# Performance work log

Hardware: AMD Instinct MI355X
Metric: run time of the kernel (lower is better)

## Reference

```python
import jax, jax.numpy as jnp
import numpy as np

EMBED_DIM = 1024
ZDIM = 128
STD = 0.02


def setup_inputs() -> dict:
    key = jax.random.key(0)
    ks = jax.random.split(key, 12)
    T, S, B, E, Z = 2048, 2048, 4, EMBED_DIM, ZDIM
    return {
        "query": jax.random.normal(ks[0], (T, B, E), jnp.float32),
        "key": jax.random.normal(ks[1], (S, B, E), jnp.float32),
        "Wq": jax.random.normal(ks[2], (2 * E + Z, E), jnp.float32) * STD,
        "bq": jnp.zeros((2 * E + Z,), jnp.float32),
        "Wk": jax.random.normal(ks[3], (Z, E), jnp.float32) * STD,
        "bk": jnp.zeros((Z,), jnp.float32),
        "Wv": jax.random.normal(ks[4], (E, E), jnp.float32) * STD,
        "bv": jnp.zeros((E,), jnp.float32),
        "Wh": jax.random.normal(ks[5], (E, E), jnp.float32) * STD,
        "bh": jnp.zeros((E,), jnp.float32),
        "gamma": jax.random.normal(ks[6], (2, Z), jnp.float32) * STD,
        "beta": jnp.zeros((2, Z), jnp.float32),
    }


def reference(query, key, Wq, bq, Wk, bk, Wv, bv, Wh, bh, gamma, beta):
    E, Z = EMBED_DIM, ZDIM
    scaling = Z ** (-0.5)
    # base: [T, B, 2E+Z]
    base = jnp.einsum('tbe,fe->tbf', query, Wq) + bq
    u = jax.nn.sigmoid(base[..., :E])                      # [T,B,E] output gate
    rq = jax.nn.silu(base[..., E:])                        # [T,B,E+Z]
    r = rq[..., :E]                                        # [T,B,E]
    q = rq[..., E:] * gamma[0] + beta[0]                   # [T,B,Z]
    k = jax.nn.silu(jnp.einsum('sbe,ze->sbz', key, Wk) + bk) * gamma[1] + beta[1]  # [S,B,Z]
    v = jax.nn.silu(jnp.einsum('sbe,fe->sbf', key, Wv) + bv)                       # [S,B,E]
    # softmax attention over context dim
    qk = jnp.einsum('tbz,sbz->bts', q * scaling, k)        # [B,T,S]
    attn = jax.nn.softmax(qk, axis=-1)
    h = jnp.einsum('bts,sbf->tbf', attn, v)                # [T,B,E]
    h = jnp.tanh(jnp.einsum('tbe,fe->tbf', h * r, Wh) + bh)
    out = query + u * (h - query)                          # addcmul
    return out
```

## Files before the change

### kernel.cpp

```cpp
#include <hip/hip_runtime.h>
#include <cstdint>
#include <cstddef>

using short8  = __attribute__((ext_vector_type(8))) short;
using floatx4 = __attribute__((ext_vector_type(4))) float;

#define DEV __device__ __forceinline__

DEV float u2f(unsigned short u){
  union { unsigned int i; float f; } c; c.i = ((unsigned int)u) << 16; return c.f;
}
DEV unsigned short f2u(float f){
  union { float f; unsigned int i; } c; c.f = f;
  unsigned int i = c.i;
  i += 0x7fffu + ((i >> 16) & 1u);
  return (unsigned short)(i >> 16);
}
DEV float sigmoidf_(float x){ return 1.0f / (1.0f + __expf(-x)); }
DEV float siluf_(float x){ return x / (1.0f + __expf(-x)); }

#define ASYNC_LD16(g, l) __builtin_amdgcn_global_load_lds( \
    (const __attribute__((address_space(1))) unsigned int*)(g), \
    (__attribute__((address_space(3))) unsigned int*)(l), 16, 0, 0)

#define MFMA_BF16 __builtin_amdgcn_mfma_f32_16x16x32_bf16

#define SBAR() asm volatile("s_barrier" ::: "memory")

constexpr float SCALING = 0.088388347648318447f;

__global__ __launch_bounds__(256) void cast_act(
    const float* __restrict__ q, const float* __restrict__ k,
    unsigned short* __restrict__ qo, unsigned short* __restrict__ ko)
{
  const int bid = blockIdx.x;
  const int e = threadIdx.x * 4;
  const float* src; unsigned short* dst;
  if (bid < 8192) {
    src = q + (long long)bid * 1024;
    dst = qo + (long long)bid * 1024;
  } else {
    const int m = bid - 8192;
    const int s = m >> 2, b = m & 3;
    src = k + (long long)m * 1024;
    dst = ko + ((long long)b * 2048 + s) * 1024;
  }
  const float4 v = *(const float4*)(src + e);
  ushort4 o; o.x=f2u(v.x); o.y=f2u(v.y); o.z=f2u(v.z); o.w=f2u(v.w);
  *(ushort4*)(dst + e) = o;
}

__global__ __launch_bounds__(256) void cast_w(
    const float* __restrict__ Wq, const float* __restrict__ Wk,
    const float* __restrict__ Wv, const float* __restrict__ Wh,
    unsigned short* __restrict__ oq, unsigned short* __restrict__ ok,
    unsigned short* __restrict__ ov, unsigned short* __restrict__ oh)
{
  const int bid = blockIdx.x;
  const int e = threadIdx.x * 4;
  const float* src; unsigned short* dst;
  if (bid < 2176)      { src = Wq + (long long)bid * 1024;        dst = oq + (long long)bid * 1024; }
  else if (bid < 2304) { src = Wk + (long long)(bid-2176) * 1024; dst = ok + (long long)(bid-2176) * 1024; }
  else if (bid < 3328) { src = Wv + (long long)(bid-2304) * 1024; dst = ov + (long long)(bid-2304) * 1024; }
  else                 { src = Wh + (long long)(bid-3328) * 1024; dst = oh + (long long)(bid-3328) * 1024; }
  const float4 v = *(const float4*)(src + e);
  ushort4 o; o.x=f2u(v.x); o.y=f2u(v.y); o.z=f2u(v.z); o.w=f2u(v.w);
  *(ushort4*)(dst + e) = o;
}

template<int EPI>
__global__ __launch_bounds__(256, 2)
void gemm_bt(const unsigned short* __restrict__ A, long long bsA, int lda,
             const unsigned short* __restrict__ Bm, long long bsB, int ldb,
             int K,
             const float* __restrict__ bias,
             const float* __restrict__ gam,
             const float* __restrict__ bet,
             float* __restrict__ f0,
             unsigned short* __restrict__ b0,
             unsigned short* __restrict__ b1,
             const unsigned short* __restrict__ rmul,
             const float* __restrict__ qin)
{
  __shared__ __align__(16) unsigned short As[128][64];
  __shared__ __align__(16) unsigned short Bs[128][64];

  const int tid = threadIdx.x;
  const int bm = blockIdx.x, bn = blockIdx.y, bz = blockIdx.z;
  const unsigned short* Ag = A  + (long long)bz * bsA;
  const unsigned short* Bg = Bm + (long long)bz * bsB;
  const int row0 = bm * 128;
  const int col0 = bn * 128;

  const int lane = tid & 63;
  const int wv   = tid >> 6;
  const int wm   = (wv & 1) * 64;
  const int wn   = (wv >> 1) * 64;
  const int lr   = lane & 15;
  const int lq   = lane >> 4;
  const int r7   = lr & 7;

  const unsigned short* gA[4]; const unsigned short* gB[4];
  unsigned short* lA[4]; unsigned short* lB[4];
  #pragma unroll
  for (int i = 0; i < 4; i++) {
    const int c  = tid + i * 256;
    const int rr = c >> 3;
    const int gc = (c & 7) ^ (rr & 7);
    gA[i] = Ag + (long long)(row0 + rr) * lda + gc * 8;
    gB[i] = Bg + (long long)(col0 + rr) * ldb + gc * 8;
    lA[i] = &As[0][0] + c * 8;
    lB[i] = &Bs[0][0] + c * 8;
  }

  floatx4 acc[4][4];
  const floatx4 zero = {0.f, 0.f, 0.f, 0.f};
  #pragma unroll
  for (int i = 0; i < 4; i++)
    #pragma unroll
    for (int j = 0; j < 4; j++) acc[i][j] = zero;

  for (int kt = 0; kt < K; kt += 64) {
    #pragma unroll
    for (int i = 0; i < 4; i++) {
      ASYNC_LD16(gA[i] + kt, lA[i]);
      ASYNC_LD16(gB[i] + kt, lB[i]);
    }
    __syncthreads();
    #pragma unroll
    for (int ks = 0; ks < 64; ks += 32) {
      const int k8 = ks >> 3;
      short8 af[4], bfv[4];
      #pragma unroll
      for (int i = 0; i < 4; i++) {
        const int sc = (lq + k8) ^ r7;
        af[i]  = *(const short8*)(&As[wm + i*16 + lr][sc * 8]);
        bfv[i] = *(const short8*)(&Bs[wn + i*16 + lr][sc * 8]);
      }
      #pragma unroll
      for (int mi = 0; mi < 4; mi++)
        #pragma unroll
        for (int ni = 0; ni < 4; ni++)
          acc[mi][ni] = MFMA_BF16(af[mi], bfv[ni], acc[mi][ni], 0, 0, 0);
    }
    __syncthreads();
  }

  #pragma unroll
  for (int mi = 0; mi < 4; mi++) {
    float s4[4];
    float iv[4];
    if constexpr (EPI == 3) {
      #pragma unroll
      for (int r = 0; r < 4; r++) s4[r] = 0.f;
    }
    if constexpr (EPI == 4) {
      #pragma unroll
      for (int r = 0; r < 4; r++) {
        const int gm = row0 + wm + mi * 16 + lq * 4 + r;
        iv[r] = 1.0f / f0[(long long)bz * 2048 + gm];
      }
    }
    #pragma unroll
    for (int ni = 0; ni < 4; ni++) {
      #pragma unroll
      for (int r = 0; r < 4; r++) {
        const int gm = row0 + wm + mi * 16 + lq * 4 + r;
        const int gn = col0 + wn + ni * 16 + lr;
        float v = acc[mi][ni][r];
        if constexpr (EPI == 2) {
          v += bias[gm];
          const int b = gn >> 11, s = gn & 2047;
          b0[((long long)b * 1024 + gm) * 2048 + s] = f2u(siluf_(v));
        } else if constexpr (EPI == 3) {
          const float e = __expf(v * SCALING);
          b0[(long long)bz * 2048 * 2048 + (long long)gm * 2048 + gn] = f2u(e);
          s4[r] += e;
        } else if constexpr (EPI == 4) {
          const long long idx = ((long long)gm * 4 + bz) * 1024 + gn;
          b0[idx] = f2u(v * iv[r] * u2f(rmul[idx]));
        } else {
          const long long idx = (long long)gm * 1024 + gn;
          const float tv = tanhf(v + bias[gn]);
          const float qv = qin[idx];
          f0[idx] = qv + u2f(rmul[idx]) * (tv - qv);
        }
      }
    }
    if constexpr (EPI == 3) {
      #pragma unroll
      for (int r = 0; r < 4; r++) {
        float s = s4[r];
        #pragma unroll
        for (int m2 = 8; m2 >= 1; m2 >>= 1) s += __shfl_xor(s, m2);
        if (lr == 0) {
          const int gm = row0 + wm + mi * 16 + lq * 4 + r;
          atomicAdd(f0 + (long long)bz * 2048 + gm, s);
        }
      }
    }
  }
}

__global__ __launch_bounds__(256, 2)
void gemm_nz128(const unsigned short* __restrict__ A0, const unsigned short* __restrict__ A1,
                const unsigned short* __restrict__ B0, const unsigned short* __restrict__ B1,
                const float* __restrict__ bi0, const float* __restrict__ bi1,
                const float* __restrict__ g0,  const float* __restrict__ g1,
                const float* __restrict__ be0, const float* __restrict__ be1,
                unsigned short* __restrict__ o0, unsigned short* __restrict__ o1)
{
  __shared__ __align__(16) unsigned short As[128][64];
  __shared__ __align__(16) unsigned short Bs[128][64];

  const int tid = threadIdx.x;
  const int bm = blockIdx.x;
  const int z  = blockIdx.z;
  const unsigned short* Ag = z ? A1 : A0;
  const unsigned short* Bg = z ? B1 : B0;
  const float* bias = z ? bi1 : bi0;
  const float* gam  = z ? g1  : g0;
  const float* bet  = z ? be1 : be0;
  unsigned short* ob = z ? o1 : o0;
  const int row0 = bm * 128;

  const int lane = tid & 63;
  const int wv   = tid >> 6;
  const int wm   = (wv & 1) * 64;
  const int wn   = (wv >> 1) * 64;
  const int lr   = lane & 15;
  const int lq   = lane >> 4;
  const int r7   = lr & 7;

  const unsigned short* gA[4]; const unsigned short* gB[4];
  unsigned short* lA[4]; unsigned short* lB[4];
  #pragma unroll
  for (int i = 0; i < 4; i++) {
    const int c  = tid + i * 256;
    const int rr = c >> 3;
    const int gc = (c & 7) ^ (rr & 7);
    gA[i] = Ag + (long long)(row0 + rr) * 1024 + gc * 8;
    gB[i] = Bg + (long long)rr * 1024 + gc * 8;
    lA[i] = &As[0][0] + c * 8;
    lB[i] = &Bs[0][0] + c * 8;
  }

  floatx4 acc[4][4];
  const floatx4 zero = {0.f, 0.f, 0.f, 0.f};
  #pragma unroll
  for (int i = 0; i < 4; i++)
    #pragma unroll
    for (int j = 0; j < 4; j++) acc[i][j] = zero;

  for (int kt = 0; kt < 1024; kt += 64) {
    #pragma unroll
    for (int i = 0; i < 4; i++) {
      ASYNC_LD16(gA[i] + kt, lA[i]);
      ASYNC_LD16(gB[i] + kt, lB[i]);
    }
    __syncthreads();
    #pragma unroll
    for (int ks = 0; ks < 64; ks += 32) {
      const int k8 = ks >> 3;
      short8 af[4], bfv[4];
      #pragma unroll
      for (int i = 0; i < 4; i++) {
        const int sc = (lq + k8) ^ r7;
        af[i]  = *(const short8*)(&As[wm + i*16 + lr][sc * 8]);
        bfv[i] = *(const short8*)(&Bs[wn + i*16 + lr][sc * 8]);
      }
      #pragma unroll
      for (int mi = 0; mi < 4; mi++)
        #pragma unroll
        for (int ni = 0; ni < 4; ni++)
          acc[mi][ni] = MFMA_BF16(af[mi], bfv[ni], acc[mi][ni], 0, 0, 0);
    }
    __syncthreads();
  }

  #pragma unroll
  for (int mi = 0; mi < 4; mi++)
    #pragma unroll
    for (int ni = 0; ni < 4; ni++)
      #pragma unroll
      for (int r = 0; r < 4; r++) {
        const int gm = row0 + wm + mi * 16 + lq * 4 + r;
        const int gn = wn + ni * 16 + lr;
        float v = acc[mi][ni][r] + bias[gn];
        ob[(long long)gm * 128 + gn] = f2u(siluf_(v) * gam[gn] + bet[gn]);
      }
}

__global__ __launch_bounds__(512, 2)
void gemm256(const unsigned short* __restrict__ A, int lda,
             const unsigned short* __restrict__ Bm, int ldb,
             int K,
             const float* __restrict__ bias,
             float* __restrict__ f0,
             unsigned short* __restrict__ b0)
{
  __shared__ __align__(16) unsigned short Ls[65536];

  const int tid = threadIdx.x;
  const int bm = blockIdx.x, bn = blockIdx.y;
  const int row0 = bm * 256;
  const int col0 = bn * 256;

  const int lane = tid & 63;
  const int wv   = tid >> 6;
  const int wr   = (wv >> 2) * 128;
  const int wc   = (wv & 3) * 64;
  const int lr   = lane & 15;
  const int lq   = lane >> 4;
  const int r7   = lr & 7;

  const int rr0 = tid >> 3;
  const int swz = ((tid & 7) ^ (rr0 & 7)) * 8;
  const unsigned short* gA0 = A  + (long long)(row0 + rr0) * lda + swz;
  const unsigned short* gB0 = Bm + (long long)(col0 + rr0) * ldb + swz;
  const long long sA64 = 64LL * lda, sB64 = 64LL * ldb;
  unsigned short* lA0 = &Ls[0]     + tid * 8;
  unsigned short* lB0 = &Ls[16384] + tid * 8;

  floatx4 acc[8][4];
  const floatx4 zero = {0.f, 0.f, 0.f, 0.f};
  #pragma unroll
  for (int i = 0; i < 8; i++)
    #pragma unroll
    for (int j = 0; j < 4; j++) acc[i][j] = zero;

  const int NT = K >> 6;

  #pragma unroll
  for (int i = 0; i < 4; i++) ASYNC_LD16(gA0 + i * sA64,      lA0 + i * 4096);
  #pragma unroll
  for (int i = 0; i < 4; i++) ASYNC_LD16(gB0 + i * sB64,      lB0 + i * 4096);
  #pragma unroll
  for (int i = 0; i < 4; i++) ASYNC_LD16(gA0 + i * sA64 + 64, lA0 + i * 4096 + 32768);
  #pragma unroll
  for (int i = 0; i < 4; i++) ASYNC_LD16(gB0 + i * sB64 + 64, lB0 + i * 4096 + 32768);
  asm volatile("s_waitcnt vmcnt(8)" ::: "memory");
  SBAR();

  for (int t = 0; t < NT; ++t) {
    const int cb = (t & 1) << 15;
    const unsigned short* Ab = &Ls[cb];
    const unsigned short* Bb = &Ls[cb + 16384];
    const bool st = (t + 2) < NT;
    const int kt2 = (t + 2) << 6;

    short8 afA[4][2], afB[4][2], bf01[2][2], bf23[2][2];

    #pragma unroll
    for (int mi = 0; mi < 4; mi++)
      #pragma unroll
      for (int k = 0; k < 2; k++)
        afA[mi][k] = *(const short8*)(Ab + (wr + mi*16 + lr) * 64 + (((k<<2) + lq) ^ r7) * 8);
    #pragma unroll
    for (int ni = 0; ni < 2; ni++)
      #pragma unroll
      for (int k = 0; k < 2; k++)
        bf01[ni][k] = *(const short8*)(Bb + (wc + ni*16 + lr) * 64 + (((k<<2) + lq) ^ r7) * 8);
    asm volatile("s_waitcnt lgkmcnt(8)" ::: "memory");
    SBAR();
    asm volatile("s_waitcnt lgkmcnt(0)" ::: "memory");
    __builtin_amdgcn_sched_barrier(0);
    __builtin_amdgcn_s_setprio(1);
    #pragma unroll
    for (int mi = 0; mi < 4; mi++)
      #pragma unroll
      for (int ni = 0; ni < 2; ni++)
        #pragma unroll
        for (int k = 0; k < 2; k++)
          acc[mi][ni] = MFMA_BF16(afA[mi][k], bf01[ni][k], acc[mi][ni], 0, 0, 0);
    __builtin_amdgcn_s_setprio(0);
    SBAR();

    #pragma unroll
    for (int ni = 0; ni < 2; ni++)
      #pragma unroll
      for (int k = 0; k < 2; k++)
        bf23[ni][k] = *(const short8*)(Bb + (wc + (ni+2)*16 + lr) * 64 + (((k<<2) + lq) ^ r7) * 8);
    SBAR();
    asm volatile("s_waitcnt lgkmcnt(0)" ::: "memory");
    __builtin_amdgcn_sched_barrier(0);
    __builtin_amdgcn_s_setprio(1);
    #pragma unroll
    for (int mi = 0; mi < 4; mi++)
      #pragma unroll
      for (int ni = 0; ni < 2; ni++)
        #pragma unroll
        for (int k = 0; k < 2; k++)
          acc[mi][ni+2] = MFMA_BF16(afA[mi][k], bf23[ni][k], acc[mi][ni+2], 0, 0, 0);
    __builtin_amdgcn_s_setprio(0);
    SBAR();

    #pragma unroll
    for (int mi = 0; mi < 4; mi++)
      #pragma unroll
      for (int k = 0; k < 2; k++)
        afB[mi][k] = *(const short8*)(Ab + (wr + (mi+4)*16 + lr) * 64 + (((k<<2) + lq) ^ r7) * 8);
    if (st) {
      #pragma unroll
      for (int i = 0; i < 4; i++) ASYNC_LD16(gB0 + i * sB64 + kt2, lB0 + i * 4096 + cb);
    }
    SBAR();
    asm volatile("s_waitcnt lgkmcnt(0)" ::: "memory");
    __builtin_amdgcn_sched_barrier(0);
    __builtin_amdgcn_s_setprio(1);
    #pragma unroll
    for (int mi = 0; mi < 4; mi++)
      #pragma unroll
      for (int ni = 0; ni < 2; ni++)
        #pragma unroll
        for (int k = 0; k < 2; k++)
          acc[mi+4][ni] = MFMA_BF16(afB[mi][k], bf01[ni][k], acc[mi+4][ni], 0, 0, 0);
    __builtin_amdgcn_s_setprio(0);
    SBAR();

    if (st) {
      #pragma unroll
      for (int i = 0; i < 4; i++) ASYNC_LD16(gA0 + i * sA64 + kt2, lA0 + i * 4096 + cb);
    }
    SBAR();
    __builtin_amdgcn_s_setprio(1);
    #pragma unroll
    for (int mi = 0; mi < 4; mi++)
      #pragma unroll
      for (int ni = 0; ni < 2; ni++)
        #pragma unroll
        for (int k = 0; k < 2; k++)
          acc[mi+4][ni+2] = MFMA_BF16(afB[mi][k], bf23[ni][k], acc[mi+4][ni+2], 0, 0, 0);
    __builtin_amdgcn_s_setprio(0);
    if (st) { asm volatile("s_waitcnt vmcnt(8)" ::: "memory"); }
    else    { asm volatile("s_waitcnt vmcnt(0)" ::: "memory"); }
    SBAR();
  }

  #pragma unroll
  for (int mi = 0; mi < 8; mi++)
    #pragma unroll
    for (int ni = 0; ni < 4; ni++)
      #pragma unroll
      for (int r = 0; r < 4; r++) {
        const int gm = row0 + wr + mi * 16 + lq * 4 + r;
        const int gn = col0 + wc + ni * 16 + lr;
        float v = acc[mi][ni][r] + bias[gn];
        if (gn < 1024) {
          ((unsigned short*)f0)[(long long)gm * 1024 + gn] = f2u(sigmoidf_(v));
        } else {
          b0[(long long)gm * 1024 + (gn - 1024)] = f2u(siluf_(v));
        }
      }
}

extern "C" void kernel_launch(void* const* d_in, const int* in_sizes, int n_in,
                              void* d_out, int out_size, void* d_ws, size_t ws_size,
                              hipStream_t stream)
{
  (void)in_sizes; (void)n_in; (void)out_size; (void)ws_size;
  const float* query = (const float*)d_in[0];
  const float* key   = (const float*)d_in[1];
  const float* Wq    = (const float*)d_in[2];
  const float* bq    = (const float*)d_in[3];
  const float* Wk    = (const float*)d_in[4];
  const float* bk    = (const float*)d_in[5];
  const float* Wv    = (const float*)d_in[6];
  const float* bv    = (const float*)d_in[7];
  const float* Wh    = (const float*)d_in[8];
  const float* bh    = (const float*)d_in[9];
  const float* gamma = (const float*)d_in[10];
  const float* beta  = (const float*)d_in[11];
  float* out = (float*)d_out;

  char* p = (char*)d_ws;
  auto take = [&](size_t bytes) -> char* {
    char* r = p; p += (bytes + 255) & ~(size_t)255; return r;
  };
  unsigned short* qbf = (unsigned short*)take(8192ULL * 1024 * 2);
  unsigned short* kbr = (unsigned short*)take(8192ULL * 1024 * 2);
  unsigned short* Wqb = (unsigned short*)take(2176ULL * 1024 * 2);
  unsigned short* Wkb = (unsigned short*)take(128ULL  * 1024 * 2);
  unsigned short* Wvb = (unsigned short*)take(1024ULL * 1024 * 2);
  unsigned short* Whb = (unsigned short*)take(1024ULL * 1024 * 2);
  unsigned short* ub  = (unsigned short*)take(8192ULL * 1024 * 2);
  unsigned short* rbf = (unsigned short*)take(8192ULL * 1024 * 2);
  unsigned short* qpj = (unsigned short*)take(8192ULL * 128 * 2);
  unsigned short* kpj = (unsigned short*)take(8192ULL * 128 * 2);
  unsigned short* vT  = (unsigned short*)take(4ULL * 1024 * 2048 * 2);
  unsigned short* Pb  = (unsigned short*)take(4ULL * 2048 * 2048 * 2);
  unsigned short* hrb = (unsigned short*)take(8192ULL * 1024 * 2);
  float*          rs  = (float*)take(4ULL * 2048 * 4);

  dim3 blk(256);
  dim3 gblk(512);
  cast_act<<<16384, blk, 0, stream>>>(query, key, qbf, kbr);
  cast_w<<<4352, blk, 0, stream>>>(Wq, Wk, Wv, Wh, Wqb, Wkb, Wvb, Whb);
  hipMemsetAsync(rs, 0, 4ULL * 2048 * 4, stream);

  gemm_nz128<<<dim3(64, 1, 2), blk, 0, stream>>>(
      qbf, kbr, Wqb + 2048LL * 1024, Wkb,
      bq + 2048, bk, gamma, gamma + 128, beta, beta + 128, qpj, kpj);
  gemm256<<<dim3(32, 8, 1), gblk, 0, stream>>>(qbf, 1024, Wqb, 1024, 1024,
      bq, (float*)ub, rbf);
  gemm_bt<2><<<dim3(8, 64, 1), blk, 0, stream>>>(Wvb, 0, 1024, kbr, 0, 1024, 1024,
      bv, nullptr, nullptr, nullptr, vT, nullptr, nullptr, nullptr);
  gemm_bt<3><<<dim3(16, 16, 4), blk, 0, stream>>>(qpj, 128, 512, kpj, 2048LL * 128, 128, 128,
      nullptr, nullptr, nullptr, rs, Pb, nullptr, nullptr, nullptr);
  gemm_bt<4><<<dim3(16, 8, 4), blk, 0, stream>>>(Pb, 2048LL * 2048, 2048,
      vT, 1024LL * 2048, 2048, 2048,
      nullptr, nullptr, nullptr, rs, hrb, nullptr, rbf, nullptr);
  gemm_bt<5><<<dim3(64, 8, 1), blk, 0, stream>>>(hrb, 0, 1024, Whb, 0, 1024, 1024,
      bh, nullptr, nullptr, out, nullptr, nullptr, ub, query);
}
```

Measured before the change: 351.8 us.

## Merge cast kernels with memset, relax launch bounds, trim barriers in gemm256

```diff
diff --git a/kernel.cpp b/kernel.cpp
--- a/kernel.cpp
+++ b/kernel.cpp
@@ -26,59 +26,54 @@
 #define MFMA_BF16 __builtin_amdgcn_mfma_f32_16x16x32_bf16
 
 #define SBAR() asm volatile("s_barrier" ::: "memory")
+#define LGKM0() asm volatile("s_waitcnt lgkmcnt(0)" ::: "memory")
 
 constexpr float SCALING = 0.088388347648318447f;
 
-__global__ __launch_bounds__(256) void cast_act(
+__global__ __launch_bounds__(256) void cast_all(
     const float* __restrict__ q, const float* __restrict__ k,
-    unsigned short* __restrict__ qo, unsigned short* __restrict__ ko)
+    const float* __restrict__ Wq, const float* __restrict__ Wk,
+    const float* __restrict__ Wv, const float* __restrict__ Wh,
+    unsigned short* __restrict__ qo, unsigned short* __restrict__ ko,
+    unsigned short* __restrict__ oq, unsigned short* __restrict__ ok,
+    unsigned short* __restrict__ ov, unsigned short* __restrict__ oh,
+    float* __restrict__ rs)
 {
   const int bid = blockIdx.x;
   const int e = threadIdx.x * 4;
+  if (bid == 20736) {
+    float4 z = {0.f, 0.f, 0.f, 0.f};
+    #pragma unroll
+    for (int i = 0; i < 8; i++)
+      *(float4*)(rs + (threadIdx.x * 8 + i) * 4) = z;
+    return;
+  }
   const float* src; unsigned short* dst;
   if (bid < 8192) {
     src = q + (long long)bid * 1024;
     dst = qo + (long long)bid * 1024;
-  } else {
+  } else if (bid < 16384) {
     const int m = bid - 8192;
     const int s = m >> 2, b = m & 3;
     src = k + (long long)m * 1024;
     dst = ko + ((long long)b * 2048 + s) * 1024;
-  }
+  } else if (bid < 18560) { src = Wq + (long long)(bid-16384) * 1024; dst = oq + (long long)(bid-16384) * 1024; }
+  else if (bid < 18688)   { src = Wk + (long long)(bid-18560) * 1024; dst = ok + (long long)(bid-18560) * 1024; }
+  else if (bid < 19712)   { src = Wv + (long long)(bid-18688) * 1024; dst = ov + (long long)(bid-18688) * 1024; }
+  else                    { src = Wh + (long long)(bid-19712) * 1024; dst = oh + (long long)(bid-19712) * 1024; }
   const float4 v = *(const float4*)(src + e);
   ushort4 o; o.x=f2u(v.x); o.y=f2u(v.y); o.z=f2u(v.z); o.w=f2u(v.w);
   *(ushort4*)(dst + e) = o;
 }
 
-__global__ __launch_bounds__(256) void cast_w(
-    const float* __restrict__ Wq, const float* __restrict__ Wk,
-    const float* __restrict__ Wv, const float* __restrict__ Wh,
-    unsigned short* __restrict__ oq, unsigned short* __restrict__ ok,
-    unsigned short* __restrict__ ov, unsigned short* __restrict__ oh)
-{
-  const int bid = blockIdx.x;
-  const int e = threadIdx.x * 4;
-  const float* src; unsigned short* dst;
-  if (bid < 2176)      { src = Wq + (long long)bid * 1024;        dst = oq + (long long)bid * 1024; }
-  else if (bid < 2304) { src = Wk + (long long)(bid-2176) * 1024; dst = ok + (long long)(bid-2176) * 1024; }
-  else if (bid < 3328) { src = Wv + (long long)(bid-2304) * 1024; dst = ov + (long long)(bid-2304) * 1024; }
-  else                 { src = Wh + (long long)(bid-3328) * 1024; dst = oh + (long long)(bid-3328) * 1024; }
-  const float4 v = *(const float4*)(src + e);
-  ushort4 o; o.x=f2u(v.x); o.y=f2u(v.y); o.z=f2u(v.z); o.w=f2u(v.w);
-  *(ushort4*)(dst + e) = o;
-}
-
 template<int EPI>
-__global__ __launch_bounds__(256, 2)
+__global__ __launch_bounds__(256, 4)
 void gemm_bt(const unsigned short* __restrict__ A, long long bsA, int lda,
              const unsigned short* __restrict__ Bm, long long bsB, int ldb,
              int K,
              const float* __restrict__ bias,
-             const float* __restrict__ gam,
-             const float* __restrict__ bet,
              float* __restrict__ f0,
              unsigned short* __restrict__ b0,
-             unsigned short* __restrict__ b1,
              const unsigned short* __restrict__ rmul,
              const float* __restrict__ qin)
 {
@@ -202,7 +197,7 @@
   }
 }
 
-__global__ __launch_bounds__(256, 2)
+__global__ __launch_bounds__(256, 4)
 void gemm_nz128(const unsigned short* __restrict__ A0, const unsigned short* __restrict__ A1,
                 const unsigned short* __restrict__ B0, const unsigned short* __restrict__ B1,
                 const float* __restrict__ bi0, const float* __restrict__ bi1,
@@ -361,10 +356,11 @@
       #pragma unroll
       for (int k = 0; k < 2; k++)
         bf01[ni][k] = *(const short8*)(Bb + (wc + ni*16 + lr) * 64 + (((k<<2) + lq) ^ r7) * 8);
-    asm volatile("s_waitcnt lgkmcnt(8)" ::: "memory");
-    SBAR();
-    asm volatile("s_waitcnt lgkmcnt(0)" ::: "memory");
-    __builtin_amdgcn_sched_barrier(0);
+    #pragma unroll
+    for (int ni = 0; ni < 2; ni++)
+      #pragma unroll
+      for (int k = 0; k < 2; k++)
+        bf23[ni][k] = *(const short8*)(Bb + (wc + (ni+2)*16 + lr) * 64 + (((k<<2) + lq) ^ r7) * 8);
     __builtin_amdgcn_s_setprio(1);
     #pragma unroll
     for (int mi = 0; mi < 4; mi++)
@@ -373,18 +369,6 @@
         #pragma unroll
         for (int k = 0; k < 2; k++)
           acc[mi][ni] = MFMA_BF16(afA[mi][k], bf01[ni][k], acc[mi][ni], 0, 0, 0);
-    __builtin_amdgcn_s_setprio(0);
-    SBAR();
-
-    #pragma unroll
-    for (int ni = 0; ni < 2; ni++)
-      #pragma unroll
-      for (int k = 0; k < 2; k++)
-        bf23[ni][k] = *(const short8*)(Bb + (wc + (ni+2)*16 + lr) * 64 + (((k<<2) + lq) ^ r7) * 8);
-    SBAR();
-    asm volatile("s_waitcnt lgkmcnt(0)" ::: "memory");
-    __builtin_amdgcn_sched_barrier(0);
-    __builtin_amdgcn_s_setprio(1);
     #pragma unroll
     for (int mi = 0; mi < 4; mi++)
       #pragma unroll
@@ -393,6 +377,7 @@
         for (int k = 0; k < 2; k++)
           acc[mi][ni+2] = MFMA_BF16(afA[mi][k], bf23[ni][k], acc[mi][ni+2], 0, 0, 0);
     __builtin_amdgcn_s_setprio(0);
+    LGKM0();
     SBAR();
 
     #pragma unroll
@@ -404,9 +389,6 @@
       #pragma unroll
       for (int i = 0; i < 4; i++) ASYNC_LD16(gB0 + i * sB64 + kt2, lB0 + i * 4096 + cb);
     }
-    SBAR();
-    asm volatile("s_waitcnt lgkmcnt(0)" ::: "memory");
-    __builtin_amdgcn_sched_barrier(0);
     __builtin_amdgcn_s_setprio(1);
     #pragma unroll
     for (int mi = 0; mi < 4; mi++)
@@ -416,13 +398,13 @@
         for (int k = 0; k < 2; k++)
           acc[mi+4][ni] = MFMA_BF16(afB[mi][k], bf01[ni][k], acc[mi+4][ni], 0, 0, 0);
     __builtin_amdgcn_s_setprio(0);
+    LGKM0();
     SBAR();
 
     if (st) {
       #pragma unroll
       for (int i = 0; i < 4; i++) ASYNC_LD16(gA0 + i * sA64 + kt2, lA0 + i * 4096 + cb);
     }
-    SBAR();
     __builtin_amdgcn_s_setprio(1);
     #pragma unroll
     for (int mi = 0; mi < 4; mi++)
@@ -494,9 +476,8 @@
 
   dim3 blk(256);
   dim3 gblk(512);
-  cast_act<<<16384, blk, 0, stream>>>(query, key, qbf, kbr);
-  cast_w<<<4352, blk, 0, stream>>>(Wq, Wk, Wv, Wh, Wqb, Wkb, Wvb, Whb);
-  hipMemsetAsync(rs, 0, 4ULL * 2048 * 4, stream);
+  cast_all<<<20737, blk, 0, stream>>>(query, key, Wq, Wk, Wv, Wh,
+      qbf, kbr, Wqb, Wkb, Wvb, Whb, rs);
 
   gemm_nz128<<<dim3(64, 1, 2), blk, 0, stream>>>(
       qbf, kbr, Wqb + 2048LL * 1024, Wkb,
@@ -504,12 +485,12 @@
   gemm256<<<dim3(32, 8, 1), gblk, 0, stream>>>(qbf, 1024, Wqb, 1024, 1024,
       bq, (float*)ub, rbf);
   gemm_bt<2><<<dim3(8, 64, 1), blk, 0, stream>>>(Wvb, 0, 1024, kbr, 0, 1024, 1024,
-      bv, nullptr, nullptr, nullptr, vT, nullptr, nullptr, nullptr);
+      bv, nullptr, vT, nullptr, nullptr);
   gemm_bt<3><<<dim3(16, 16, 4), blk, 0, stream>>>(qpj, 128, 512, kpj, 2048LL * 128, 128, 128,
-      nullptr, nullptr, nullptr, rs, Pb, nullptr, nullptr, nullptr);
+      nullptr, rs, Pb, nullptr, nullptr);
   gemm_bt<4><<<dim3(16, 8, 4), blk, 0, stream>>>(Pb, 2048LL * 2048, 2048,
       vT, 1024LL * 2048, 2048, 2048,
-      nullptr, nullptr, nullptr, rs, hrb, nullptr, rbf, nullptr);
+      nullptr, rs, hrb, rbf, nullptr);
   gemm_bt<5><<<dim3(64, 8, 1), blk, 0, stream>>>(hrb, 0, 1024, Whb, 0, 1024, 1024,
-      bh, nullptr, nullptr, out, nullptr, nullptr, ub, query);
-}
+      bh, out, nullptr, ub, query);
+}
```

New measurement: 472.7 us. 34.4% more time.
